# Optimization experiments

Measured on AMD Instinct MI355X. Metric: run time of the kernel, lower is better.

Reference implementation:

```python
import jax, jax.numpy as jnp
import numpy as np

ETA = 0.5
R_CUTOFF = 6.0
ZETA = 0.6
LAMDA = 0.8
RS = 1.0
SPECIAL_ATOM = 8  # atom index routed to elem2 net


def _af(x):
    return 1.0 / (1.0 + x * x)


def _mlp(g, w1, b1, w2, b2, w3, b3):
    h = _af(g @ w1.T + b1)
    h = _af(h @ w2.T + b2)
    return h @ w3.T + b3  # [N,1]


def setup_inputs() -> dict:
    key = jax.random.key(0)
    ks = jax.random.split(key, 13)
    N = 384
    x = jax.random.normal(ks[0], (N, 3), dtype=jnp.float32) * 2.0
    def lin(kw, kb, fout, fin):
        w = jax.random.normal(kw, (fout, fin), dtype=jnp.float32) * (1.0 / np.sqrt(fin))
        b = jax.random.normal(kb, (fout,), dtype=jnp.float32) * 0.1
        return w, b
    w1a, b1a = lin(ks[1], ks[2], 40, 2)
    w2a, b2a = lin(ks[3], ks[4], 40, 40)
    w3a, b3a = lin(ks[5], ks[6], 1, 40)
    w1b, b1b = lin(ks[7], ks[8], 40, 2)
    w2b, b2b = lin(ks[9], ks[10], 40, 40)
    w3b, b3b = lin(ks[11], ks[12], 1, 40)
    return {"x": x,
            "w1a": w1a, "b1a": b1a, "w2a": w2a, "b2a": b2a, "w3a": w3a, "b3a": b3a,
            "w1b": w1b, "b1b": b1b, "w2b": w2b, "b2b": b2b, "w3b": w3b, "b3b": b3b}


def _descriptors(x):
    N = x.shape[0]
    eye = jnp.eye(N, dtype=bool)
    diff = x[:, None, :] - x[None, :, :]           # [N,N,3]
    D2 = jnp.sum(diff * diff, axis=-1)             # [N,N]
    D = jnp.sqrt(jnp.where(eye, 1.0, D2))
    D = jnp.where(eye, 0.0, D)
    # cutoff function (hard 0 beyond R_cutoff), zeroed on diagonal
    fc = jnp.where((D <= R_CUTOFF) & (~eye), 0.5 * (jnp.cos(np.pi * D / R_CUTOFF) + 1.0), 0.0)
    # radial symmetry function per atom i
    rad = jnp.sum(jnp.exp(-ETA * (D - RS) ** 2) * fc, axis=1)  # [N]
    # angular: sum over triplets j<k, j!=i, k!=i
    A = jnp.exp(-ETA * D2) * fc                    # [N,N], zero on diagonal
    Gm = x @ x.T                                   # Gram matrix
    gd = jnp.diag(Gm)
    # dot(Rij, Rki) with Rij = x_i - x_j, Rki = x_k - x_i
    dot = Gm[:, None, :] - gd[:, None, None] - Gm[None, :, :] + Gm[:, :, None]  # [N,N,N] (i,j,k)
    denom = D[:, :, None] * D[:, None, :]          # |Rij| * |Rki|
    cos_theta = dot / jnp.where(denom > 0, denom, 1.0)
    term1 = jnp.maximum(1.0 + LAMDA * cos_theta, 1e-6) ** ZETA
    # A[i,j] * A[j,k] * A[k,i]; diag-zero A kills i==j and i==k terms
    term2 = A[:, :, None] * A[None, :, :] * A[:, None, :]
    tri = jnp.triu(jnp.ones((N, N), dtype=jnp.float32), k=1)[None, :, :]  # j < k
    ang = (2.0 ** (1.0 - ZETA)) * jnp.sum(term1 * term2 * tri, axis=(1, 2))  # [N]
    return jnp.stack([ang, rad], axis=-1)          # [N,2], order matches Gi=[ang, rad]


def reference(x, w1a, b1a, w2a, b2a, w3a, b3a, w1b, b1b, w2b, b2b, w3b, b3b):
    G = _descriptors(x)
    q1 = _mlp(G, w1a, b1a, w2a, b2a, w3a, b3a)[:, 0]
    q2 = _mlp(G, w1b, b1b, w2b, b2b, w3b, b3b)[:, 0]
    idx = jnp.arange(x.shape[0])
    return jnp.where(idx == SPECIAL_ATOM, q2, q1)  # [N]
```

## Files before the change

### kernel.cpp

```cpp
#include <hip/hip_runtime.h>
#include <math.h>

#define N 384
#define EPSA 1e-4f

#if __has_builtin(__builtin_amdgcn_logf) && __has_builtin(__builtin_amdgcn_exp2f)
#define LOG2F(x) __builtin_amdgcn_logf(x)
#define EXP2F(x) __builtin_amdgcn_exp2f(x)
#else
#define LOG2F(x) __log2f(x)
#define EXP2F(x) __expf(0.69314718056f * (x))
#endif

__device__ __forceinline__ float wave_reduce(float v) {
#pragma unroll
    for (int o = 32; o > 0; o >>= 1) v += __shfl_down(v, o, 64);
    return v;
}

__global__ __launch_bounds__(128) void pair_kernel(
    const float* __restrict__ x, float* __restrict__ A,
    float4* __restrict__ nbr4, int* __restrict__ nbrJ, int* __restrict__ cnt,
    float* __restrict__ rad, float* __restrict__ ang) {
    const int i = blockIdx.x;
    const int t = threadIdx.x;
    const int lane = t & 63, w = t >> 6;
    const float xi0 = x[3 * i + 0], xi1 = x[3 * i + 1], xi2 = x[3 * i + 2];

    float racc = 0.0f;
    float4 val[3];
    int keep[3];
#pragma unroll
    for (int r = 0; r < 3; ++r) {
        const int j = t + 128 * r;
        float dx = xi0 - x[3 * j + 0];
        float dy = xi1 - x[3 * j + 1];
        float dz = xi2 - x[3 * j + 2];
        float d2 = dx * dx + dy * dy + dz * dz;
        float a = 0.0f, rr = 0.0f, inv = 0.0f;
        if (j != i) {
            float d = sqrtf(d2);
            if (d <= 6.0f) {
                float fc = 0.5f * (__cosf(0.52359877559829887f * d) + 1.0f);
                a = __expf(-0.5f * d2) * fc;
                float dm = d - 1.0f;
                rr = __expf(-0.5f * dm * dm) * fc;
            }
            inv = rsqrtf(d2);
        }
        A[i * N + j] = a;
        racc += rr;
        val[r] = make_float4(dx * inv, dy * inv, dz * inv, a);
        keep[r] = (a > EPSA) ? 1 : 0;
    }

    __shared__ int bcnt[6], bbase[6], realn;
    int pfx[3];
#pragma unroll
    for (int r = 0; r < 3; ++r) {
        unsigned long long m = __ballot(keep[r]);
        pfx[r] = __popcll(m & ((1ull << lane) - 1ull));
        if (lane == 0) bcnt[w + 2 * r] = __popcll(m);
    }
    __syncthreads();
    if (t == 0) {
        int s = 0;
#pragma unroll
        for (int c = 0; c < 6; ++c) { bbase[c] = s; s += bcnt[c]; }
        realn = s;
        cnt[i] = (s + 7) & ~7;
        ang[i] = 0.0f;
    }
    __syncthreads();
#pragma unroll
    for (int r = 0; r < 3; ++r) {
        if (keep[r]) {
            const int slot = bbase[w + 2 * r] + pfx[r];
            nbr4[i * N + slot] = val[r];
            nbrJ[i * N + slot] = t + 128 * r;
        }
    }
    const int rn = realn;
    const int np = (rn + 7) & ~7;
    if (t < np - rn) {
        nbr4[i * N + rn + t] = make_float4(0.f, 0.f, 0.f, 0.f);
        nbrJ[i * N + rn + t] = i;
    }

    __shared__ float red[2];
    float v = wave_reduce(racc);
    if (lane == 0) red[w] = v;
    __syncthreads();
    if (t == 0) rad[i] = red[0] + red[1];
}

__global__ __launch_bounds__(256) void ang_kernel(
    const float* __restrict__ A, const float4* __restrict__ nbr4,
    const int* __restrict__ nbrJ, const int* __restrict__ cnt,
    float* __restrict__ ang) {
    const int i = blockIdx.x;
    const int jc = blockIdx.y;
    const int t = threadIdx.x;
    const int n = cnt[i];
    if (n == 0) return;
    const int iN = i * N;
    const int nb = n >> 3;

    float acc = 0.0f;
    for (int ks0 = 0; ks0 < n; ks0 += 256) {
        const int ks = ks0 + t;
        const bool valid = ks < n;
        float4 K = valid ? nbr4[iN + ks] : make_float4(0.f, 0.f, 0.f, 0.f);
        const int kcol = valid ? nbrJ[iN + ks] : 0;
        const float kx = -0.8f * K.x, ky = -0.8f * K.y, kz = -0.8f * K.z;
        const float kA = K.w;
        const float* Acol = A + kcol;

        float cacc = 0.0f;
        for (int b = jc; b < nb; b += 4) {
            const int s0 = b << 3;
            float a8[8];
#pragma unroll
            for (int q = 0; q < 8; ++q)
                a8[q] = Acol[nbrJ[iN + s0 + q] * N];
#pragma unroll
            for (int q = 0; q < 8; ++q) {
                float4 J = nbr4[iN + s0 + q];
                float bb = fmaf(J.x, kx, fmaf(J.y, ky, fmaf(J.z, kz, 1.0f)));
                float p = EXP2F(0.6f * LOG2F(bb));
                cacc = fmaf(J.w * a8[q], p, cacc);
            }
        }
        acc = fmaf(kA, cacc, acc);
    }

    __shared__ float red[4];
    float v = wave_reduce(acc);
    if ((t & 63) == 0) red[t >> 6] = v;
    __syncthreads();
    if (t == 0) atomicAdd(&ang[i], red[0] + red[1] + red[2] + red[3]);
}

#define WSTRIDE 1804
__global__ __launch_bounds__(64) void mlp_kernel(
    const float* __restrict__ ang, const float* __restrict__ rad,
    float* __restrict__ out,
    const float* w1a, const float* b1a, const float* w2a, const float* b2a,
    const float* w3a, const float* b3a, const float* w1b, const float* b1b,
    const float* w2b, const float* b2b, const float* w3b, const float* b3b) {
    __shared__ __align__(16) float W[2 * WSTRIDE];
    const int t = threadIdx.x;
    {
        const float* srcs[12] = {w1a, b1a, w2a, b2a, w3a, b3a,
                                 w1b, b1b, w2b, b2b, w3b, b3b};
        const int ns[6] = {80, 40, 1600, 40, 40, 1};
        const int offs[6] = {0, 80, 120, 1720, 1760, 1800};
        for (int s = 0; s < 12; ++s) {
            const int base = (s / 6) * WSTRIDE + offs[s % 6];
            const int n4 = ns[s % 6] >> 2;
            const float4* src4 = (const float4*)srcs[s];
            float4* dst4 = (float4*)(W + base);
            for (int q = t; q < n4; q += 64) dst4[q] = src4[q];
        }
        if (t == 0) {
            W[1800] = b3a[0];
            W[WSTRIDE + 1800] = b3b[0];
        }
    }
    __syncthreads();

    const int atom = blockIdx.x * 16 + (t >> 2);
    const int net = (t >> 1) & 1;
    const int half = t & 1;
    const float* P = W + net * WSTRIDE;

    const float g0 = 0.6597539553864471f * ang[atom];
    const float g1 = rad[atom];

    float h1[40];
#pragma unroll
    for (int u = 0; u < 40; ++u) {
        float z = fmaf(P[2 * u], g0, fmaf(P[2 * u + 1], g1, P[80 + u]));
        h1[u] = 1.0f / fmaf(z, z, 1.0f);
    }

    float acc = half ? 0.0f : P[1800];
    const int v0 = half * 20;
    for (int v2 = v0; v2 < v0 + 20; ++v2) {
        const float4* row = (const float4*)(P + 120 + v2 * 40);
        float z0 = P[1720 + v2], z1 = 0.0f, z2 = 0.0f, z3 = 0.0f;
#pragma unroll
        for (int q = 0; q < 10; ++q) {
            float4 r = row[q];
            z0 = fmaf(r.x, h1[4 * q + 0], z0);
            z1 = fmaf(r.y, h1[4 * q + 1], z1);
            z2 = fmaf(r.z, h1[4 * q + 2], z2);
            z3 = fmaf(r.w, h1[4 * q + 3], z3);
        }
        float z = (z0 + z1) + (z2 + z3);
        float h = 1.0f / fmaf(z, z, 1.0f);
        acc = fmaf(P[1760 + v2], h, acc);
    }
    acc += __shfl_down(acc, 1, 64);

    if (half == 0 && net == ((atom == 8) ? 1 : 0)) out[atom] = acc;
}

extern "C" void kernel_launch(void* const* d_in, const int* in_sizes, int n_in,
                              void* d_out, int out_size, void* d_ws, size_t ws_size,
                              hipStream_t stream) {
    const float* x = (const float*)d_in[0];
    const float* w1a = (const float*)d_in[1];
    const float* b1a = (const float*)d_in[2];
    const float* w2a = (const float*)d_in[3];
    const float* b2a = (const float*)d_in[4];
    const float* w3a = (const float*)d_in[5];
    const float* b3a = (const float*)d_in[6];
    const float* w1b = (const float*)d_in[7];
    const float* b1b = (const float*)d_in[8];
    const float* w2b = (const float*)d_in[9];
    const float* b2b = (const float*)d_in[10];
    const float* w3b = (const float*)d_in[11];
    const float* b3b = (const float*)d_in[12];
    float* out = (float*)d_out;

    float* ws = (float*)d_ws;
    float* A = ws;
    float4* nbr4 = (float4*)(ws + 147456);
    int* nbrJ = (int*)(ws + 147456 + 4 * 147456);
    float* rad = ws + 147456 * 6;
    float* ang = rad + 384;
    int* cnt = (int*)(ang + 384);

    hipLaunchKernelGGL(pair_kernel, dim3(N), dim3(128), 0, stream,
                       x, A, nbr4, nbrJ, cnt, rad, ang);
    hipLaunchKernelGGL(ang_kernel, dim3(N, 4), dim3(256), 0, stream,
                       A, nbr4, nbrJ, cnt, ang);
    hipLaunchKernelGGL(mlp_kernel, dim3(24), dim3(64), 0, stream,
                       ang, rad, out,
                       w1a, b1a, w2a, b2a, w3a, b3a,
                       w1b, b1b, w2b, b2b, w3b, b3b);
}
```

Before: 111.0 us.

## Exploit j<k symmetry in angular sum and fuse MLP into last angular block

The angular kernel now visits only j blocks at or after the k thread's block, masks pairs with j<=k, and doubles the descriptor scale instead of summing all ordered pairs. This roughly halves the triplet work. The separate MLP launch is removed: the last of two blocks per atom, found through a done counter and atomics, evaluates both small MLPs for that atom. The neighbour cutoff EPSA is raised, dropping more weak neighbours, which adds approximation error.

```diff
diff --git a/kernel.cpp b/kernel.cpp
--- a/kernel.cpp
+++ b/kernel.cpp
@@ -2,7 +2,7 @@
 #include <math.h>
 
 #define N 384
-#define EPSA 1e-4f
+#define EPSA 4e-4f
 
 #if __has_builtin(__builtin_amdgcn_logf) && __has_builtin(__builtin_amdgcn_exp2f)
 #define LOG2F(x) __builtin_amdgcn_logf(x)
@@ -21,7 +21,7 @@
 __global__ __launch_bounds__(128) void pair_kernel(
     const float* __restrict__ x, float* __restrict__ A,
     float4* __restrict__ nbr4, int* __restrict__ nbrJ, int* __restrict__ cnt,
-    float* __restrict__ rad, float* __restrict__ ang) {
+    float* __restrict__ rad, float* __restrict__ ang, int* __restrict__ done) {
     const int i = blockIdx.x;
     const int t = threadIdx.x;
     const int lane = t & 63, w = t >> 6;
@@ -70,6 +70,7 @@
         realn = s;
         cnt[i] = (s + 7) & ~7;
         ang[i] = 0.0f;
+        done[i] = 0;
     }
     __syncthreads();
 #pragma unroll
@@ -97,12 +98,18 @@
 __global__ __launch_bounds__(256) void ang_kernel(
     const float* __restrict__ A, const float4* __restrict__ nbr4,
     const int* __restrict__ nbrJ, const int* __restrict__ cnt,
-    float* __restrict__ ang) {
+    const float* __restrict__ rad, float* __restrict__ ang,
+    int* __restrict__ done, float* __restrict__ out,
+    const float* __restrict__ w1a, const float* __restrict__ b1a,
+    const float* __restrict__ w2a, const float* __restrict__ b2a,
+    const float* __restrict__ w3a, const float* __restrict__ b3a,
+    const float* __restrict__ w1b, const float* __restrict__ b1b,
+    const float* __restrict__ w2b, const float* __restrict__ b2b,
+    const float* __restrict__ w3b, const float* __restrict__ b3b) {
     const int i = blockIdx.x;
     const int jc = blockIdx.y;
     const int t = threadIdx.x;
     const int n = cnt[i];
-    if (n == 0) return;
     const int iN = i * N;
     const int nb = n >> 3;
 
@@ -116,8 +123,10 @@
         const float kA = K.w;
         const float* Acol = A + kcol;
 
+        const int bw = ((ks0 >> 3) + ((t >> 6) << 3)) + jc;
+
         float cacc = 0.0f;
-        for (int b = jc; b < nb; b += 4) {
+        for (int b = bw; b < nb; b += 2) {
             const int s0 = b << 3;
             float a8[8];
 #pragma unroll
@@ -128,82 +137,64 @@
                 float4 J = nbr4[iN + s0 + q];
                 float bb = fmaf(J.x, kx, fmaf(J.y, ky, fmaf(J.z, kz, 1.0f)));
                 float p = EXP2F(0.6f * LOG2F(bb));
-                cacc = fmaf(J.w * a8[q], p, cacc);
+                float aw = (s0 + q > ks) ? a8[q] : 0.0f;
+                cacc = fmaf(J.w * aw, p, cacc);
             }
         }
         acc = fmaf(kA, cacc, acc);
     }
 
     __shared__ float red[4];
+    __shared__ int s_win;
+    __shared__ float s_ang;
     float v = wave_reduce(acc);
     if ((t & 63) == 0) red[t >> 6] = v;
     __syncthreads();
-    if (t == 0) atomicAdd(&ang[i], red[0] + red[1] + red[2] + red[3]);
-}
-
-#define WSTRIDE 1804
-__global__ __launch_bounds__(64) void mlp_kernel(
-    const float* __restrict__ ang, const float* __restrict__ rad,
-    float* __restrict__ out,
-    const float* w1a, const float* b1a, const float* w2a, const float* b2a,
-    const float* w3a, const float* b3a, const float* w1b, const float* b1b,
-    const float* w2b, const float* b2b, const float* w3b, const float* b3b) {
-    __shared__ __align__(16) float W[2 * WSTRIDE];
-    const int t = threadIdx.x;
-    {
-        const float* srcs[12] = {w1a, b1a, w2a, b2a, w3a, b3a,
-                                 w1b, b1b, w2b, b2b, w3b, b3b};
-        const int ns[6] = {80, 40, 1600, 40, 40, 1};
-        const int offs[6] = {0, 80, 120, 1720, 1760, 1800};
-        for (int s = 0; s < 12; ++s) {
-            const int base = (s / 6) * WSTRIDE + offs[s % 6];
-            const int n4 = ns[s % 6] >> 2;
-            const float4* src4 = (const float4*)srcs[s];
-            float4* dst4 = (float4*)(W + base);
-            for (int q = t; q < n4; q += 64) dst4[q] = src4[q];
-        }
-        if (t == 0) {
-            W[1800] = b3a[0];
-            W[WSTRIDE + 1800] = b3b[0];
-        }
-    }
-    __syncthreads();
-
-    const int atom = blockIdx.x * 16 + (t >> 2);
-    const int net = (t >> 1) & 1;
-    const int half = t & 1;
-    const float* P = W + net * WSTRIDE;
-
-    const float g0 = 0.6597539553864471f * ang[atom];
-    const float g1 = rad[atom];
-
-    float h1[40];
-#pragma unroll
-    for (int u = 0; u < 40; ++u) {
-        float z = fmaf(P[2 * u], g0, fmaf(P[2 * u + 1], g1, P[80 + u]));
-        h1[u] = 1.0f / fmaf(z, z, 1.0f);
-    }
-
-    float acc = half ? 0.0f : P[1800];
-    const int v0 = half * 20;
-    for (int v2 = v0; v2 < v0 + 20; ++v2) {
-        const float4* row = (const float4*)(P + 120 + v2 * 40);
-        float z0 = P[1720 + v2], z1 = 0.0f, z2 = 0.0f, z3 = 0.0f;
-#pragma unroll
-        for (int q = 0; q < 10; ++q) {
-            float4 r = row[q];
-            z0 = fmaf(r.x, h1[4 * q + 0], z0);
-            z1 = fmaf(r.y, h1[4 * q + 1], z1);
-            z2 = fmaf(r.z, h1[4 * q + 2], z2);
-            z3 = fmaf(r.w, h1[4 * q + 3], z3);
-        }
-        float z = (z0 + z1) + (z2 + z3);
+    if (t == 0) {
+        float s = red[0] + red[1] + red[2] + red[3];
+        atomicAdd(&ang[i], s);
+        __threadfence();
+        int old = atomicAdd(&done[i], 1);
+        s_win = (old == 1);
+        if (old == 1) s_ang = atomicAdd(&ang[i], 0.0f);
+    }
+    __syncthreads();
+    if (!s_win) return;
+
+    __shared__ float h1s[2][40];
+    __shared__ float contrib[80];
+    const float g0 = 1.3195079107728942f * s_ang;
+    const float g1 = rad[i];
+
+    if (t < 80) {
+        const int net = t / 40, u = t - net * 40;
+        const float* w1 = net ? w1b : w1a;
+        const float* b1 = net ? b1b : b1a;
+        float z = fmaf(w1[2 * u], g0, fmaf(w1[2 * u + 1], g1, b1[u]));
+        h1s[net][u] = 1.0f / fmaf(z, z, 1.0f);
+    }
+    __syncthreads();
+    if (t < 80) {
+        const int net = t / 40, vv = t - net * 40;
+        const float* w2 = net ? w2b : w2a;
+        const float* b2 = net ? b2b : b2a;
+        const float* w3 = net ? w3b : w3a;
+        const float* row = w2 + vv * 40;
+        float z = b2[vv];
+#pragma unroll 8
+        for (int u = 0; u < 40; ++u) z = fmaf(row[u], h1s[net][u], z);
         float h = 1.0f / fmaf(z, z, 1.0f);
-        acc = fmaf(P[1760 + v2], h, acc);
-    }
-    acc += __shfl_down(acc, 1, 64);
-
-    if (half == 0 && net == ((atom == 8) ? 1 : 0)) out[atom] = acc;
+        contrib[t] = w3[vv] * h;
+    }
+    __syncthreads();
+    if (t < 2) {
+        const float* b3 = t ? b3b : b3a;
+        float q = b3[0];
+        for (int vv = 0; vv < 40; ++vv) q += contrib[t * 40 + vv];
+        contrib[t] = q;
+    }
+    __syncthreads();
+    if (t == 0) out[i] = (i == 8) ? contrib[1] : contrib[0];
 }
 
 extern "C" void kernel_launch(void* const* d_in, const int* in_sizes, int n_in,
@@ -231,13 +222,12 @@
     float* rad = ws + 147456 * 6;
     float* ang = rad + 384;
     int* cnt = (int*)(ang + 384);
+    int* done = cnt + 384;
 
     hipLaunchKernelGGL(pair_kernel, dim3(N), dim3(128), 0, stream,
-                       x, A, nbr4, nbrJ, cnt, rad, ang);
-    hipLaunchKernelGGL(ang_kernel, dim3(N, 4), dim3(256), 0, stream,
-                       A, nbr4, nbrJ, cnt, ang);
-    hipLaunchKernelGGL(mlp_kernel, dim3(24), dim3(64), 0, stream,
-                       ang, rad, out,
+                       x, A, nbr4, nbrJ, cnt, rad, ang, done);
+    hipLaunchKernelGGL(ang_kernel, dim3(N, 2), dim3(256), 0, stream,
+                       A, nbr4, nbrJ, cnt, rad, ang, done, out,
                        w1a, b1a, w2a, b2a, w3a, b3a,
                        w1b, b1b, w2b, b2b, w3b, b3b);
 }
```

Result: faster. 102.3 us (-7.9%).
